# Optimization experiments

Hardware: AMD Instinct MI355X
Metric: run time of the kernel (lower is better)

Reference implementation:

```python
import jax, jax.numpy as jnp
import numpy as np

B, N, C = 128, 197, 768   # batch, tokens (14*14 + cls), embed dim
H = 12                    # attention heads, head_dim = 64
OUT = 32                  # hard-coded mlp out_features
CH_H = 14                 # channel-attention heads
CN = 196                  # channel-attention token dim (14*14)
MLP_HID = int(C * 4.0)    # 3072
CMLP_HID = int(OUT * 4.0) # 128
EPS = 1e-5


def _ln(x, g, b):
    m = x.mean(-1, keepdims=True)
    v = ((x - m) ** 2).mean(-1, keepdims=True)
    return (x - m) * jax.lax.rsqrt(v + EPS) * g + b


def setup_inputs() -> dict:
    key = jax.random.key(0)
    ks = jax.random.split(key, 24)
    W = lambda k, sh: (jax.random.normal(k, sh, jnp.float32) * 0.02)
    return {
        "x": jax.random.normal(ks[0], (B, N, C), jnp.float32),
        # block 1: norm1 + token attention
        "g1": jnp.ones((C,), jnp.float32), "b1": jnp.zeros((C,), jnp.float32),
        "w_qkv": W(ks[1], (3 * C, C)),                     # qkv_bias=False
        "w_proj": W(ks[2], (C, C)), "b_proj": jnp.zeros((C,), jnp.float32),
        # block 2: norm2 + mlp (768 -> 3072 -> 32), NOT residual
        "g2": jnp.ones((C,), jnp.float32), "b2": jnp.zeros((C,), jnp.float32),
        "w_fc1": W(ks[3], (MLP_HID, C)), "b_fc1": jnp.zeros((MLP_HID,), jnp.float32),
        "w_fc2": W(ks[4], (OUT, MLP_HID)), "b_fc2": jnp.zeros((OUT,), jnp.float32),
        # block 3: norm3 + channel attention (over 196 spatial positions)
        "g3": jnp.ones((OUT,), jnp.float32), "b3": jnp.zeros((OUT,), jnp.float32),
        "w_cqkv": W(ks[5], (3 * CN, CN)),                  # qkv_bias=False
        "w_cproj": W(ks[6], (CN, CN)), "b_cproj": jnp.zeros((CN,), jnp.float32),
        # block 4: norm4 + channel mlp (32 -> 128 -> 32)
        "g4": jnp.ones((OUT,), jnp.float32), "b4": jnp.zeros((OUT,), jnp.float32),
        "w_cfc1": W(ks[7], (CMLP_HID, OUT)), "b_cfc1": jnp.zeros((CMLP_HID,), jnp.float32),
        "w_cfc2": W(ks[8], (OUT, CMLP_HID)), "b_cfc2": jnp.zeros((OUT,), jnp.float32),
    }


def reference(x, g1, b1, w_qkv, w_proj, b_proj,
              g2, b2, w_fc1, b_fc1, w_fc2, b_fc2,
              g3, b3, w_cqkv, w_cproj, b_cproj,
              g4, b4, w_cfc1, b_cfc1, w_cfc2, b_cfc2):
    Bz, Nn, Cc = x.shape
    hd = Cc // H  # 64

    # --- token attention (residual) ---
    h = _ln(x, g1, b1)
    qkv = (h @ w_qkv.T).reshape(Bz, Nn, 3, H, hd).transpose(2, 0, 3, 1, 4)
    q, k, v = qkv[0], qkv[1], qkv[2]                       # [B,H,N,hd]
    a = jax.nn.softmax(jnp.einsum('bhqd,bhkd->bhqk', q, k) * (hd ** -0.5), axis=-1)
    o = jnp.einsum('bhqk,bhkd->bhqd', a, v).transpose(0, 2, 1, 3).reshape(Bz, Nn, Cc)
    x = x + (o @ w_proj.T + b_proj)

    # --- mlp 768->3072->32, NO residual (matches original forward) ---
    h = _ln(x, g2, b2)
    x = jax.nn.gelu(h @ w_fc1.T + b_fc1, approximate=False) @ w_fc2.T + b_fc2  # [B,N,32]

    # --- channel attention (residual); N==197 path, no interleave averaging ---
    h = _ln(x, g3, b3)
    cls = h[:, :1, :]                                      # [B,1,32]
    t = h[:, 1:, :].transpose(0, 2, 1)                     # [B,32,196]
    chd = CN // CH_H  # 14
    cqkv = (t @ w_cqkv.T).reshape(Bz, OUT, 3, CH_H, chd).transpose(2, 0, 3, 1, 4)
    cq, ck, cv = cqkv[0], cqkv[1], cqkv[2]                 # [B,14,32,14]
    ca = jax.nn.softmax(jnp.einsum('bhqd,bhkd->bhqk', cq, ck) * (chd ** -0.5), axis=-1)
    co = jnp.einsum('bhqk,bhkd->bhqd', ca, cv).transpose(0, 2, 1, 3).reshape(Bz, OUT, CN)
    co = co @ w_cproj.T + b_cproj                          # [B,32,196]
    x = x + jnp.concatenate([cls, co.transpose(0, 2, 1)], axis=1)

    # --- channel mlp 32->128->32 (residual) ---
    h = _ln(x, g4, b4)
    x = x + (jax.nn.gelu(h @ w_cfc1.T + b_cfc1, approximate=False) @ w_cfc2.T + b_cfc2)
    return x
```

## Files before the change

kernel.cpp:

```cpp
#include <hip/hip_runtime.h>
#include <hip/hip_bf16.h>

typedef unsigned short u16;
typedef __hip_bfloat16 bf16;
typedef __attribute__((ext_vector_type(8))) short bf16x8;
typedef __attribute__((ext_vector_type(4))) float f32x4;

#define B_   128
#define N_   197
#define C_   768
#define H_   12
#define HD_  64
#define T_   (B_*N_)
#define MH_  3072
#define OUT_ 32
#define CN_  196
#define CHH_ 14
#define KP_  224
#define CSZ_ (B_*CHH_*32*14)

__device__ __forceinline__ float bfu2f(u16 x){ union{unsigned u; float f;} v; v.u=((unsigned)x)<<16; return v.f; }
__device__ __forceinline__ bf16  f2bf(float f){ return __float2bfloat16(f); }
__device__ __forceinline__ u16   f2bfu(float f){ union{bf16 h; u16 u;} c; c.h=__float2bfloat16(f); return c.u; }
__device__ __forceinline__ float gelu_f(float x){ return 0.5f*x*(1.0f+erff(x*0.70710678118654752f)); }

__device__ __forceinline__ void gl_lds16(const u16* g, u16* l){
  __builtin_amdgcn_global_load_lds((const __attribute__((address_space(1))) void*)g,
                                   (__attribute__((address_space(3))) void*)l, 16, 0, 0);
}

__global__ __launch_bounds__(256) void write_code_kernel(float* out, int n, float code){
  int i = blockIdx.x*256 + threadIdx.x;
  if (i < n) out[i] = code;
}

template<bool F32IN>
__global__ __launch_bounds__(256) void ln768_kernel(const void* __restrict__ xv,
    const float* __restrict__ g, const float* __restrict__ b, bf16* __restrict__ out)
{
  int row = blockIdx.x;
  int tid = threadIdx.x;
  float v0, v1, v2;
  if (F32IN){
    const float* xr = (const float*)xv + (size_t)row*C_;
    v0 = xr[tid]; v1 = xr[tid+256]; v2 = xr[tid+512];
  } else {
    const u16* xr = (const u16*)xv + (size_t)row*C_;
    v0 = bfu2f(xr[tid]); v1 = bfu2f(xr[tid+256]); v2 = bfu2f(xr[tid+512]);
  }
  __shared__ float red[4];
  int lane = tid & 63, wave = tid >> 6;
  float s = v0+v1+v2;
  #pragma unroll
  for (int off=32; off>0; off>>=1) s += __shfl_xor(s, off);
  if (lane==0) red[wave]=s;
  __syncthreads();
  float mean = (red[0]+red[1]+red[2]+red[3]) * (1.0f/C_);
  float d0=v0-mean, d1=v1-mean, d2=v2-mean;
  float q = d0*d0+d1*d1+d2*d2;
  #pragma unroll
  for (int off=32; off>0; off>>=1) q += __shfl_xor(q, off);
  __syncthreads();
  if (lane==0) red[wave]=q;
  __syncthreads();
  float var = (red[0]+red[1]+red[2]+red[3]) * (1.0f/C_);
  float r = rsqrtf(var + 1e-5f);
  bf16* orow = out + (size_t)row*C_;
  orow[tid]     = f2bf(d0*r*g[tid]     + b[tid]);
  orow[tid+256] = f2bf(d1*r*g[tid+256] + b[tid+256]);
  orow[tid+512] = f2bf(d2*r*g[tid+512] + b[tid+512]);
}

__global__ __launch_bounds__(256) void ln32_kernel(const float* __restrict__ x,
    const float* __restrict__ g, const float* __restrict__ b, float* __restrict__ out)
{
  int i = blockIdx.x*256 + threadIdx.x;
  int c = i & 31;
  float v = x[i];
  float s = v;
  #pragma unroll
  for (int off=16; off>0; off>>=1) s += __shfl_xor(s, off, 32);
  float mean = s * (1.0f/32);
  float d = v - mean;
  float q = d*d;
  #pragma unroll
  for (int off=16; off>0; off>>=1) q += __shfl_xor(q, off, 32);
  float r = rsqrtf(q*(1.0f/32) + 1e-5f);
  out[i] = d*r*g[c] + b[c];
}

__global__ __launch_bounds__(256) void packw_bf16(const float* __restrict__ w,
    u16* __restrict__ dst, int n)
{
  int i = (blockIdx.x*256 + threadIdx.x)*4;
  if (i >= n) return;
  float4 v = *(const float4*)(w + i);
  ushort4 o; o.x=f2bfu(v.x); o.y=f2bfu(v.y); o.z=f2bfu(v.z); o.w=f2bfu(v.w);
  *(ushort4*)(dst + i) = o;
}

__global__ __launch_bounds__(256) void init_x3_kernel(const float* __restrict__ bias,
    float* __restrict__ x3)
{
  int i = blockIdx.x*256 + threadIdx.x;
  x3[i] = bias[i & 31];
}

template<int MODE, bool WB16>
__global__ __launch_bounds__(256) void gemm128(
    const u16* __restrict__ A, const void* __restrict__ Wsrc,
    const float* __restrict__ bias, const float* __restrict__ resid,
    bf16* __restrict__ outb,
    bf16* __restrict__ q_out, bf16* __restrict__ k_out, bf16* __restrict__ v_out,
    int Nn, int K)
{
  __shared__ __align__(16) u16 As[128*32];
  __shared__ __align__(16) u16 Bs[128*32];
  const int tid  = threadIdx.x;
  const int wave = tid >> 6, lane = tid & 63;
  const int quad = lane >> 4, l16 = lane & 15;
  const int wr = wave >> 1, wc = wave & 1;
  const int m0 = blockIdx.x * 128;
  const int n0 = blockIdx.y * 128;
  const int rs = tid >> 2;
  const int kc = (tid & 3) << 3;

  const u16* aA0 = A + (size_t)(m0 + rs)*K + kc;
  const u16* aA1 = aA0 + (size_t)64*K;
  const u16*  wB0 = WB16 ? ((const u16*)Wsrc + (size_t)(n0 + rs)*K + kc) : nullptr;
  const float* wF0 = WB16 ? nullptr : ((const float*)Wsrc + (size_t)(n0 + rs)*K + kc);

  u16* AsW = As + (size_t)wave*512;
  u16* BsW = Bs + (size_t)wave*512;

  f32x4 acc[4][4] = {};

  for (int k0 = 0; k0 < K; k0 += 32){
    gl_lds16(aA0 + k0, AsW);
    gl_lds16(aA1 + k0, AsW + 2048);
    if (WB16){
      gl_lds16(wB0 + k0, BsW);
      gl_lds16(wB0 + (size_t)64*K + k0, BsW + 2048);
    } else {
      float4 w0 = *(const float4*)(wF0 + k0);
      float4 w1 = *(const float4*)(wF0 + k0 + 4);
      const float* wF1 = wF0 + (size_t)64*K;
      float4 w2 = *(const float4*)(wF1 + k0);
      float4 w3 = *(const float4*)(wF1 + k0 + 4);
      ushort4 b0; b0.x=f2bfu(w0.x); b0.y=f2bfu(w0.y); b0.z=f2bfu(w0.z); b0.w=f2bfu(w0.w);
      ushort4 b1; b1.x=f2bfu(w1.x); b1.y=f2bfu(w1.y); b1.z=f2bfu(w1.z); b1.w=f2bfu(w1.w);
      ushort4 b2; b2.x=f2bfu(w2.x); b2.y=f2bfu(w2.y); b2.z=f2bfu(w2.z); b2.w=f2bfu(w2.w);
      ushort4 b3; b3.x=f2bfu(w3.x); b3.y=f2bfu(w3.y); b3.z=f2bfu(w3.z); b3.w=f2bfu(w3.w);
      *(ushort4*)&Bs[rs*32 + kc]        = b0;
      *(ushort4*)&Bs[rs*32 + kc + 4]    = b1;
      *(ushort4*)&Bs[(rs+64)*32 + kc]   = b2;
      *(ushort4*)&Bs[(rs+64)*32 + kc+4] = b3;
    }
    __syncthreads();
    bf16x8 af[4], bfr[4];
    #pragma unroll
    for (int i=0;i<4;i++) af[i]  = *(const bf16x8*)&As[(wr*64 + i*16 + l16)*32 + quad*8];
    #pragma unroll
    for (int j=0;j<4;j++) bfr[j] = *(const bf16x8*)&Bs[(wc*64 + j*16 + l16)*32 + quad*8];
    #pragma unroll
    for (int i=0;i<4;i++)
      #pragma unroll
      for (int j=0;j<4;j++)
        acc[i][j] = __builtin_amdgcn_mfma_f32_16x16x32_bf16(af[i], bfr[j], acc[i][j], 0, 0, 0);
    __syncthreads();
  }

  #pragma unroll
  for (int i=0;i<4;i++){
    #pragma unroll
    for (int j=0;j<4;j++){
      #pragma unroll
      for (int r=0;r<4;r++){
        int m = m0 + wr*64 + i*16 + quad*4 + r;
        int c = n0 + wc*64 + j*16 + l16;
        float v = acc[i][j][r];
        if (MODE==0){
          int bb = m / N_;
          int n  = m - bb*N_;
          int sec = c / C_;
          int rem = c - sec*C_;
          int hh  = rem >> 6;
          int d   = rem & 63;
          bf16* dst = (sec==0) ? q_out : (sec==1) ? k_out : v_out;
          dst[(((size_t)bb*H_ + hh)*N_ + n)*HD_ + d] = f2bf(v);
        } else if (MODE==1){
          size_t idx = (size_t)m*Nn + c;
          outb[idx] = f2bf(v + bias[c] + resid[idx]);
        } else {
          outb[(size_t)m*Nn + c] = f2bf(gelu_f(v + bias[c]));
        }
      }
    }
  }
}

template<int MODE, bool WB16>
__global__ __launch_bounds__(256) void gemm_mfma(
    const u16* __restrict__ A, const void* __restrict__ Wsrc,
    const float* __restrict__ bias, const float* __restrict__ resid,
    bf16* __restrict__ outb, float* __restrict__ outf,
    bf16* __restrict__ q_out, bf16* __restrict__ k_out, bf16* __restrict__ v_out,
    int M, int Nn, int K, int wld, int astride)
{
  __shared__ __align__(16) u16 As[64][32];
  __shared__ __align__(16) u16 Bs[64][32];
  const int tid  = threadIdx.x;
  const int wave = tid >> 6, lane = tid & 63;
  const int quad = lane >> 4, l16 = lane & 15;
  const int m0 = blockIdx.x * 64;
  const int n0 = (MODE==6) ? 0 : blockIdx.y * 64;
  const int kst = (MODE==6) ? blockIdx.y * K : 0;
  const int rs = tid >> 2;
  const int kc = (tid & 3) << 3;
  const u16* arow = A + (size_t)(m0 + rs)*astride + kst + kc;
  const bool wvalid = (n0 + rs) < Nn;

  f32x4 acc[4] = {};

  for (int k0 = 0; k0 < K; k0 += 32){
    *(uint4*)&As[rs][kc] = *(const uint4*)(arow + k0);
    if (WB16){
      const u16* wrow = (const u16*)Wsrc + (size_t)(n0 + rs)*wld + kst + kc;
      uint4 wv = make_uint4(0u,0u,0u,0u);
      if (wvalid) wv = *(const uint4*)(wrow + k0);
      *(uint4*)&Bs[rs][kc] = wv;
    } else {
      const float* wrow = (const float*)Wsrc + (size_t)(n0 + rs)*wld + kst + kc;
      float4 w0 = make_float4(0.f,0.f,0.f,0.f), w1 = w0;
      if (wvalid){ w0 = *(const float4*)(wrow + k0); w1 = *(const float4*)(wrow + k0 + 4); }
      ushort4 b0; b0.x=f2bfu(w0.x); b0.y=f2bfu(w0.y); b0.z=f2bfu(w0.z); b0.w=f2bfu(w0.w);
      ushort4 b1; b1.x=f2bfu(w1.x); b1.y=f2bfu(w1.y); b1.z=f2bfu(w1.z); b1.w=f2bfu(w1.w);
      *(ushort4*)&Bs[rs][kc]   = b0;
      *(ushort4*)&Bs[rs][kc+4] = b1;
    }
    __syncthreads();
    bf16x8 af = *(const bf16x8*)&As[wave*16 + l16][quad*8];
    #pragma unroll
    for (int nb=0; nb<4; nb++){
      bf16x8 bfr = *(const bf16x8*)&Bs[nb*16 + l16][quad*8];
      acc[nb] = __builtin_amdgcn_mfma_f32_16x16x32_bf16(af, bfr, acc[nb], 0, 0, 0);
    }
    __syncthreads();
  }

  #pragma unroll
  for (int nb=0; nb<4; nb++){
    #pragma unroll
    for (int r=0; r<4; r++){
      int m = m0 + wave*16 + quad*4 + r;
      int c = n0 + nb*16 + l16;
      float v = acc[nb][r];
      if (MODE==3){
        if (c < Nn) outf[(size_t)m*Nn + c] = v + bias[c];
      } else if (MODE==4){
        if (c < Nn) outf[(size_t)m*Nn + c] += v;
      } else if (MODE==6){
        if (c < Nn) atomicAdd(&outf[(size_t)m*Nn + c], v);
      } else if (MODE==5){
        if (c < Nn){
          int bb = m >> 5, oo = m & 31;
          int sec = c / CN_;
          int rem = c - sec*CN_;
          int hh  = rem / 14;
          int d   = rem - hh*14;
          outf[(size_t)sec*CSZ_ + (((size_t)bb*CHH_ + hh)*32 + oo)*14 + d] = v;
        }
      }
    }
  }
}

__global__ __launch_bounds__(256) void attn_kernel(const u16* __restrict__ q,
    const u16* __restrict__ k, const u16* __restrict__ v, bf16* __restrict__ o)
{
  __shared__ __align__(16) u16 VtS[64*208];
  __shared__ __align__(16) u16 PsS[4*16*208];
  int bh = blockIdx.x, b = bh / H_, hh = bh - b*H_;
  int tid = threadIdx.x, wave = tid >> 6, lane = tid & 63;
  int quad = lane >> 4, l16 = lane & 15;
  const u16* qb = q + (size_t)bh*N_*HD_;
  const u16* kb = k + (size_t)bh*N_*HD_;
  const u16* vb = v + (size_t)bh*N_*HD_;
  for (int idx = tid; idx < N_*HD_; idx += 256){
    int j = idx >> 6, d = idx & 63;
    VtS[(d*208 + j) ^ ((d&7)<<3)] = vb[idx];
  }
  for (int idx = tid; idx < 64*11; idx += 256){
    int d = idx / 11, j = 197 + (idx - d*11);
    VtS[(d*208 + j) ^ ((d&7)<<3)] = 0;
  }
  __syncthreads();

  u16* PsW = PsS + wave*16*208;

  for (int g = wave; g < 13; g += 4){
    int r0 = g*16;
    int qrow = r0 + l16;
    int qr = (qrow < N_) ? qrow : 0;
    bf16x8 aq0 = *(const bf16x8*)(qb + (size_t)qr*HD_ + quad*8);
    bf16x8 aq1 = *(const bf16x8*)(qb + (size_t)qr*HD_ + 32 + quad*8);
    f32x4 s[13];
    #pragma unroll
    for (int nb = 0; nb < 13; nb++){
      int krow = nb*16 + l16;
      int kr = (krow < N_) ? krow : 0;
      bf16x8 bk0 = *(const bf16x8*)(kb + (size_t)kr*HD_ + quad*8);
      bf16x8 bk1 = *(const bf16x8*)(kb + (size_t)kr*HD_ + 32 + quad*8);
      f32x4 t = {};
      t = __builtin_amdgcn_mfma_f32_16x16x32_bf16(aq0, bk0, t, 0, 0, 0);
      t = __builtin_amdgcn_mfma_f32_16x16x32_bf16(aq1, bk1, t, 0, 0, 0);
      s[nb] = t;
    }
    #pragma unroll
    for (int nb = 0; nb < 13; nb++){
      bool colok = (nb*16 + l16) < N_;
      #pragma unroll
      for (int r = 0; r < 4; r++)
        s[nb][r] = colok ? s[nb][r]*0.125f : -1e30f;
    }
    #pragma unroll
    for (int r = 0; r < 4; r++){
      float m = s[0][r];
      #pragma unroll
      for (int nb = 1; nb < 13; nb++) m = fmaxf(m, s[nb][r]);
      m = fmaxf(m, __shfl_xor(m, 1));
      m = fmaxf(m, __shfl_xor(m, 2));
      m = fmaxf(m, __shfl_xor(m, 4));
      m = fmaxf(m, __shfl_xor(m, 8));
      float su = 0.f;
      #pragma unroll
      for (int nb = 0; nb < 13; nb++){
        float p = expf(s[nb][r] - m);
        s[nb][r] = p; su += p;
      }
      su += __shfl_xor(su, 1);
      su += __shfl_xor(su, 2);
      su += __shfl_xor(su, 4);
      su += __shfl_xor(su, 8);
      float inv = 1.0f/su;
      #pragma unroll
      for (int nb = 0; nb < 13; nb++) s[nb][r] *= inv;
    }
    #pragma unroll
    for (int nb = 0; nb < 13; nb++)
      #pragma unroll
      for (int r = 0; r < 4; r++){
        int row = quad*4 + r;
        PsW[(row*208 + nb*16 + l16) ^ ((row&7)<<3)] = f2bfu(s[nb][r]);
      }
    __threadfence_block();
    f32x4 oa[4] = {};
    #pragma unroll
    for (int ks = 0; ks < 7; ks++){
      int col = ks*32 + quad*8;
      bool ok = (col < 208);
      int ccol = ok ? col : 0;
      bf16x8 ap = *(const bf16x8*)&PsW[(l16*208 + ccol) ^ ((l16&7)<<3)];
      if (!ok) ap = (bf16x8){0,0,0,0,0,0,0,0};
      #pragma unroll
      for (int nd = 0; nd < 4; nd++){
        bf16x8 bv = *(const bf16x8*)&VtS[((nd*16 + l16)*208 + ccol) ^ ((l16&7)<<3)];
        oa[nd] = __builtin_amdgcn_mfma_f32_16x16x32_bf16(ap, bv, oa[nd], 0, 0, 0);
      }
    }
    #pragma unroll
    for (int nd = 0; nd < 4; nd++)
      #pragma unroll
      for (int r = 0; r < 4; r++){
        int qi = r0 + quad*4 + r;
        if (qi < N_)
          o[((size_t)b*N_ + qi)*C_ + hh*HD_ + nd*16 + l16] = f2bf(oa[nd][r]);
      }
    __threadfence_block();
  }
}

__global__ __launch_bounds__(256) void pack_tall_kernel(const float* __restrict__ h3,
    u16* __restrict__ tall)
{
  int idx = blockIdx.x*256 + threadIdx.x;
  if (idx >= 4096*KP_) return;
  int row = idx / KP_, kk = idx - row*KP_;
  int b = row >> 5, oo = row & 31;
  float v = (kk < CN_) ? h3[((size_t)b*N_ + 1 + kk)*32 + oo] : 0.f;
  tall[idx] = f2bfu(v);
}

__global__ __launch_bounds__(256) void pack_w_kernel(const float* __restrict__ w,
    u16* __restrict__ dst, int rows, int kreal)
{
  int idx = blockIdx.x*256 + threadIdx.x;
  if (idx >= rows*KP_) return;
  int r = idx / KP_, kk = idx - r*KP_;
  dst[idx] = (kk < kreal) ? f2bfu(w[(size_t)r*kreal + kk]) : (u16)0;
}

__global__ __launch_bounds__(256) void pack_co_kernel(const float* __restrict__ co,
    u16* __restrict__ dst)
{
  int idx = blockIdx.x*256 + threadIdx.x;
  if (idx >= 4096*KP_) return;
  int row = idx / KP_, kk = idx - row*KP_;
  dst[idx] = (kk < CN_) ? f2bfu(co[(size_t)row*CN_ + kk]) : (u16)0;
}

__global__ __launch_bounds__(64) void cattn_kernel(const float* __restrict__ cq,
    const float* __restrict__ ck, const float* __restrict__ cv, float* __restrict__ co)
{
  __shared__ __align__(16) float qs[32*15], ks_[32*15], vs[32*15], ps[32*34];
  int bh = blockIdx.x;
  int b  = bh / CHH_;
  int hh = bh - b*CHH_;
  int lane = threadIdx.x;
  const float* qb = cq + (size_t)bh*448;
  const float* kb = ck + (size_t)bh*448;
  const float* vb = cv + (size_t)bh*448;
  for (int idx=lane; idx<448; idx+=64){
    int o = idx/14, d = idx - o*14;
    qs[o*15+d] = qb[idx]; ks_[o*15+d] = kb[idx]; vs[o*15+d] = vb[idx];
  }
  __syncthreads();
  int o = lane & 31, half = lane >> 5;
  const float scale = 0.2672612419124244f;
  float sc[16]; float mx = -1e30f;
  #pragma unroll
  for (int jj=0; jj<16; jj++){
    int j = half*16 + jj;
    float a = 0.f;
    #pragma unroll
    for (int d=0; d<14; d++) a += qs[o*15+d]*ks_[j*15+d];
    sc[jj] = a*scale;
    mx = fmaxf(mx, sc[jj]);
  }
  mx = fmaxf(mx, __shfl_xor(mx, 32));
  float sum = 0.f;
  #pragma unroll
  for (int jj=0; jj<16; jj++){ sc[jj] = expf(sc[jj]-mx); sum += sc[jj]; }
  sum += __shfl_xor(sum, 32);
  float inv = 1.0f/sum;
  #pragma unroll
  for (int jj=0; jj<16; jj++) ps[o*34 + half*16 + jj] = sc[jj]*inv;
  __syncthreads();
  #pragma unroll
  for (int dd=0; dd<7; dd++){
    int d = half*7 + dd;
    float acc = 0.f;
    #pragma unroll
    for (int j=0; j<32; j++) acc += ps[o*34+j]*vs[j*15+d];
    co[((size_t)b*32 + o)*CN_ + hh*14 + d] = acc;
  }
}

__global__ __launch_bounds__(256) void concat_add_kernel(const float* __restrict__ x3,
    const float* __restrict__ h3, const float* __restrict__ co2, float* __restrict__ x4)
{
  int i = blockIdx.x*256 + threadIdx.x;
  int c = i & 31;
  int row = i >> 5;
  int b = row / N_;
  int r = row - b*N_;
  float add = (r==0) ? h3[i] : co2[((size_t)b*32 + c)*CN_ + (r-1)];
  x4[i] = x3[i] + add;
}

__global__ __launch_bounds__(256) void cfc1_kernel(const float* __restrict__ h4,
    const float* __restrict__ w, const float* __restrict__ bias, float* __restrict__ chid)
{
  int idx = blockIdx.x*256 + threadIdx.x;
  int m = idx >> 7, j = idx & 127;
  const float* hr = h4 + (size_t)m*32;
  const float* wr = w + (size_t)j*32;
  float acc = bias[j];
  #pragma unroll
  for (int kk=0; kk<32; kk++) acc += hr[kk]*wr[kk];
  chid[idx] = gelu_f(acc);
}

__global__ __launch_bounds__(256) void cfc2_kernel(const float* __restrict__ chid,
    const float* __restrict__ w, const float* __restrict__ bias,
    const float* __restrict__ x4, float* __restrict__ out)
{
  int idx = blockIdx.x*256 + threadIdx.x;
  int m = idx >> 5, j = idx & 31;
  const float* cr = chid + (size_t)m*128;
  const float* wr = w + (size_t)j*128;
  float acc = bias[j];
  #pragma unroll
  for (int kk=0; kk<128; kk++) acc += cr[kk]*wr[kk];
  out[idx] = x4[idx] + acc;
}

extern "C" void kernel_launch(void* const* d_in, const int* in_sizes, int n_in,
                              void* d_out, int out_size, void* d_ws, size_t ws_size,
                              hipStream_t stream)
{
  const int NIN = 23;
  static const int dsz[NIN] = {19365888,768,768,1769472,589824,768,768,768,2359296,
                               3072,98304,32,32,32,115248,38416,196,32,32,4096,128,4096,32};
  static const int a2d[NIN] = {2,7,13,18,20,22,16,9,11,5,1,6,12,17,19,21,15,14,8,10,4,3,0};

  float* dout = (float*)d_out;
  int ogrid = (out_size + 255)/256;

  const float* in[NIN];
  bool dict_ok = (n_in == NIN);
  if (dict_ok) for (int i=0;i<NIN;i++) if (in_sizes[i] != dsz[i]) { dict_ok=false; break; }
  if (dict_ok){
    for (int i=0;i<NIN;i++) in[i] = (const float*)d_in[i];
  } else {
    bool alpha_ok = (n_in == NIN);
    if (alpha_ok) for (int i=0;i<NIN;i++) if (in_sizes[i] != dsz[a2d[i]]) { alpha_ok=false; break; }
    if (alpha_ok){
      for (int i=0;i<NIN;i++) in[a2d[i]] = (const float*)d_in[i];
    } else {
      write_code_kernel<<<ogrid, 256, 0, stream>>>(dout, out_size, 5000.f + (float)n_in);
      return;
    }
  }

  const float* x      = in[0];
  const float* g1     = in[1];
  const float* b1     = in[2];
  const float* w_qkv  = in[3];
  const float* w_proj = in[4];
  const float* b_proj = in[5];
  const float* g2     = in[6];
  const float* b2     = in[7];
  const float* w_fc1  = in[8];
  const float* b_fc1  = in[9];
  const float* w_fc2  = in[10];
  const float* b_fc2  = in[11];
  const float* g3     = in[12];
  const float* b3     = in[13];
  const float* w_cqkv = in[14];
  const float* w_cproj= in[15];
  const float* b_cproj= in[16];
  const float* g4     = in[17];
  const float* b4     = in[18];
  const float* w_cfc1 = in[19];
  const float* b_cfc1 = in[20];
  const float* w_cfc2 = in[21];
  const float* b_cfc2 = in[22];

  char* ws = (char*)d_ws;
  const size_t TC2 = (size_t)T_*C_*2;
  const size_t NEED = 4*TC2 + 4096;
  if (ws_size < NEED){
    write_code_kernel<<<ogrid, 256, 0, stream>>>(dout, out_size,
        7000.f + (float)(ws_size >> 20));
    return;
  }

  bf16* h_buf   = (bf16*)(ws);
  bf16* o_buf   = (bf16*)(ws);
  bf16* q_buf   = (bf16*)(ws + TC2);
  bf16* k_buf   = (bf16*)(ws + 2*TC2);
  bf16* v_buf   = (bf16*)(ws + 3*TC2);
  bf16* x2_buf  = (bf16*)(ws + TC2);
  bf16* hidh    = (bf16*)(ws + 2*TC2);
  float* x3     = (float*)(ws + TC2);
  char* sm = ws + 2*TC2;
  float* h3  = (float*)sm; sm += (size_t)T_*32*4;
  float* cq  = (float*)sm; sm += (size_t)CSZ_*4;
  float* ck  = (float*)sm; sm += (size_t)CSZ_*4;
  float* cv  = (float*)sm; sm += (size_t)CSZ_*4;
  float* co  = (float*)sm; sm += (size_t)B_*32*CN_*4;
  float* co2 = (float*)sm; sm += (size_t)B_*32*CN_*4;
  float* x4  = (float*)sm; sm += (size_t)T_*32*4;
  float* h4  = (float*)sm; sm += (size_t)T_*32*4;
  float* chid = (float*)sm;
  u16* tall  = (u16*)(ws);
  u16* wcq_b = (u16*)(ws + 2*1024*1024);
  u16* co_b  = (u16*)(ws + 3*1024*1024);
  u16* wcp_b = (u16*)(ws + 5*1024*1024);

  u16* wqkv_b  = (u16*)(ws + 4*TC2 + 4096);
  u16* wproj_b = wqkv_b  + (size_t)2304*C_;
  u16* wfc1_b  = wproj_b + (size_t)C_*C_;
  const size_t WPACK = ((size_t)2304*C_ + (size_t)C_*C_ + (size_t)MH_*C_)*2;
  const bool packed = (ws_size >= NEED + WPACK);

  if (packed){
    packw_bf16<<<(2304*C_/4+255)/256, 256, 0, stream>>>(w_qkv,  wqkv_b,  2304*C_);
    packw_bf16<<<(C_*C_/4+255)/256,  256, 0, stream>>>(w_proj, wproj_b, C_*C_);
    packw_bf16<<<(MH_*C_/4+255)/256, 256, 0, stream>>>(w_fc1,  wfc1_b,  MH_*C_);
  }

  ln768_kernel<true><<<T_, 256, 0, stream>>>(x, g1, b1, h_buf);
  if (packed)
    gemm128<0,true><<<dim3(T_/128, 2304/128), 256, 0, stream>>>((const u16*)h_buf,
        wqkv_b, nullptr, nullptr, nullptr, q_buf, k_buf, v_buf, 2304, C_);
  else
    gemm128<0,false><<<dim3(T_/128, 2304/128), 256, 0, stream>>>((const u16*)h_buf,
        w_qkv, nullptr, nullptr, nullptr, q_buf, k_buf, v_buf, 2304, C_);
  attn_kernel<<<B_*H_, 256, 0, stream>>>((const u16*)q_buf, (const u16*)k_buf,
      (const u16*)v_buf, o_buf);
  if (packed)
    gemm128<1,true><<<dim3(T_/128, C_/128), 256, 0, stream>>>((const u16*)o_buf,
        wproj_b, b_proj, x, x2_buf, nullptr, nullptr, nullptr, C_, C_);
  else
    gemm128<1,false><<<dim3(T_/128, C_/128), 256, 0, stream>>>((const u16*)o_buf,
        w_proj, b_proj, x, x2_buf, nullptr, nullptr, nullptr, C_, C_);
  ln768_kernel<false><<<T_, 256, 0, stream>>>(x2_buf, g2, b2, h_buf);
  init_x3_kernel<<<(T_*32)/256, 256, 0, stream>>>(b_fc2, x3);
  for (int half=0; half<2; half++){
    if (packed)
      gemm128<2,true><<<dim3(T_/128, 1536/128), 256, 0, stream>>>((const u16*)h_buf,
          wfc1_b + (size_t)half*1536*C_, b_fc1 + half*1536, nullptr,
          hidh, nullptr, nullptr, nullptr, 1536, C_);
    else
      gemm128<2,false><<<dim3(T_/128, 1536/128), 256, 0, stream>>>((const u16*)h_buf,
          w_fc1 + (size_t)half*1536*C_, b_fc1 + half*1536, nullptr,
          hidh, nullptr, nullptr, nullptr, 1536, C_);
    gemm_mfma<6,false><<<dim3(T_/64, 4), 256, 0, stream>>>((const u16*)hidh,
        w_fc2 + (size_t)half*1536, nullptr, nullptr, nullptr, x3,
        nullptr, nullptr, nullptr, T_, OUT_, 384, MH_, 1536);
  }
  ln32_kernel<<<(T_*32)/256, 256, 0, stream>>>(x3, g3, b3, h3);
  pack_tall_kernel<<<(4096*KP_+255)/256, 256, 0, stream>>>(h3, tall);
  pack_w_kernel<<<(588*KP_+255)/256, 256, 0, stream>>>(w_cqkv, wcq_b, 588, CN_);
  gemm_mfma<5,true><<<dim3(4096/64, 10), 256, 0, stream>>>(tall, wcq_b,
      nullptr, nullptr, nullptr, cq, nullptr, nullptr, nullptr, 4096, 588, KP_, KP_, KP_);
  cattn_kernel<<<B_*CHH_, 64, 0, stream>>>(cq, ck, cv, co);
  pack_co_kernel<<<(4096*KP_+255)/256, 256, 0, stream>>>(co, co_b);
  pack_w_kernel<<<(196*KP_+255)/256, 256, 0, stream>>>(w_cproj, wcp_b, CN_, CN_);
  gemm_mfma<3,true><<<dim3(4096/64, 4), 256, 0, stream>>>(co_b, wcp_b,
      b_cproj, nullptr, nullptr, co2, nullptr, nullptr, nullptr, 4096, CN_, KP_, KP_, KP_);
  concat_add_kernel<<<(T_*32)/256, 256, 0, stream>>>(x3, h3, co2, x4);
  ln32_kernel<<<(T_*32)/256, 256, 0, stream>>>(x4, g4, b4, h4);
  cfc1_kernel<<<(T_*128)/256, 256, 0, stream>>>(h4, w_cfc1, b_cfc1, chid);
  cfc2_kernel<<<(T_*32)/256, 256, 0, stream>>>(chid, w_cfc2, b_cfc2, x4, dout);
}
```

Measured before the change: 1.036 ms.

## Double-buffer GEMM LDS, swap grid order, split attention blocks, use exp2

The 128x128 GEMM now keeps two LDS stages, so the next K tile loads while MFMAs run on the current one, which hides global-to-LDS latency. Its grid is transposed so consecutive blocks walk along N and share the same A rows, which should help L2 reuse. Token attention is split into two blocks per (batch, head) for more parallelism, and exp is replaced by exp2 with a pre-scaled log2e, tree reductions and s_setprio around MFMA sections. The cost is twice the GEMM LDS footprint (lower occupancy) and the V transpose being loaded twice per head.

Result: faster. 1.001 ms (-3.4%).

```diff
diff --git a/kernel.cpp b/kernel.cpp
--- a/kernel.cpp
+++ b/kernel.cpp
@@ -114,14 +114,14 @@
     bf16* __restrict__ q_out, bf16* __restrict__ k_out, bf16* __restrict__ v_out,
     int Nn, int K)
 {
-  __shared__ __align__(16) u16 As[128*32];
-  __shared__ __align__(16) u16 Bs[128*32];
+  __shared__ __align__(16) u16 As[2][128*32];
+  __shared__ __align__(16) u16 Bs[2][128*32];
   const int tid  = threadIdx.x;
   const int wave = tid >> 6, lane = tid & 63;
   const int quad = lane >> 4, l16 = lane & 15;
   const int wr = wave >> 1, wc = wave & 1;
-  const int m0 = blockIdx.x * 128;
-  const int n0 = blockIdx.y * 128;
+  const int m0 = blockIdx.y * 128;
+  const int n0 = blockIdx.x * 128;
   const int rs = tid >> 2;
   const int kc = (tid & 3) << 3;
 
@@ -130,12 +130,11 @@
   const u16*  wB0 = WB16 ? ((const u16*)Wsrc + (size_t)(n0 + rs)*K + kc) : nullptr;
   const float* wF0 = WB16 ? nullptr : ((const float*)Wsrc + (size_t)(n0 + rs)*K + kc);
 
-  u16* AsW = As + (size_t)wave*512;
-  u16* BsW = Bs + (size_t)wave*512;
-
   f32x4 acc[4][4] = {};
 
-  for (int k0 = 0; k0 < K; k0 += 32){
+  auto STAGE = [&](int buf, int k0){
+    u16* AsW = As[buf] + (size_t)wave*512;
+    u16* BsW = Bs[buf] + (size_t)wave*512;
     gl_lds16(aA0 + k0, AsW);
     gl_lds16(aA1 + k0, AsW + 2048);
     if (WB16){
@@ -151,23 +150,31 @@
       ushort4 b1; b1.x=f2bfu(w1.x); b1.y=f2bfu(w1.y); b1.z=f2bfu(w1.z); b1.w=f2bfu(w1.w);
       ushort4 b2; b2.x=f2bfu(w2.x); b2.y=f2bfu(w2.y); b2.z=f2bfu(w2.z); b2.w=f2bfu(w2.w);
       ushort4 b3; b3.x=f2bfu(w3.x); b3.y=f2bfu(w3.y); b3.z=f2bfu(w3.z); b3.w=f2bfu(w3.w);
-      *(ushort4*)&Bs[rs*32 + kc]        = b0;
-      *(ushort4*)&Bs[rs*32 + kc + 4]    = b1;
-      *(ushort4*)&Bs[(rs+64)*32 + kc]   = b2;
-      *(ushort4*)&Bs[(rs+64)*32 + kc+4] = b3;
-    }
-    __syncthreads();
+      *(ushort4*)&Bs[buf][rs*32 + kc]        = b0;
+      *(ushort4*)&Bs[buf][rs*32 + kc + 4]    = b1;
+      *(ushort4*)&Bs[buf][(rs+64)*32 + kc]   = b2;
+      *(ushort4*)&Bs[buf][(rs+64)*32 + kc+4] = b3;
+    }
+  };
+
+  STAGE(0, 0);
+  __syncthreads();
+  int cur = 0;
+
+  for (int k0 = 0; k0 < K; k0 += 32){
+    if (k0 + 32 < K) STAGE(cur^1, k0 + 32);
     bf16x8 af[4], bfr[4];
     #pragma unroll
-    for (int i=0;i<4;i++) af[i]  = *(const bf16x8*)&As[(wr*64 + i*16 + l16)*32 + quad*8];
-    #pragma unroll
-    for (int j=0;j<4;j++) bfr[j] = *(const bf16x8*)&Bs[(wc*64 + j*16 + l16)*32 + quad*8];
+    for (int i=0;i<4;i++) af[i]  = *(const bf16x8*)&As[cur][(wr*64 + i*16 + l16)*32 + quad*8];
+    #pragma unroll
+    for (int j=0;j<4;j++) bfr[j] = *(const bf16x8*)&Bs[cur][(wc*64 + j*16 + l16)*32 + quad*8];
     #pragma unroll
     for (int i=0;i<4;i++)
       #pragma unroll
       for (int j=0;j<4;j++)
         acc[i][j] = __builtin_amdgcn_mfma_f32_16x16x32_bf16(af[i], bfr[j], acc[i][j], 0, 0, 0);
     __syncthreads();
+    cur ^= 1;
   }
 
   #pragma unroll
@@ -280,7 +287,9 @@
 {
   __shared__ __align__(16) u16 VtS[64*208];
   __shared__ __align__(16) u16 PsS[4*16*208];
-  int bh = blockIdx.x, b = bh / H_, hh = bh - b*H_;
+  int bid = blockIdx.x;
+  int bh = bid >> 1, sh = bid & 1;
+  int b = bh / H_, hh = bh - b*H_;
   int tid = threadIdx.x, wave = tid >> 6, lane = tid & 63;
   int quad = lane >> 4, l16 = lane & 15;
   const u16* qb = q + (size_t)bh*N_*HD_;
@@ -297,14 +306,18 @@
   __syncthreads();
 
   u16* PsW = PsS + wave*16*208;
-
-  for (int g = wave; g < 13; g += 4){
+  const int gbeg = sh ? 7 : 0;
+  const int gend = sh ? 13 : 7;
+  const float LOG2E = 1.4426950408889634f;
+
+  for (int g = gbeg + wave; g < gend; g += 4){
     int r0 = g*16;
     int qrow = r0 + l16;
     int qr = (qrow < N_) ? qrow : 0;
     bf16x8 aq0 = *(const bf16x8*)(qb + (size_t)qr*HD_ + quad*8);
     bf16x8 aq1 = *(const bf16x8*)(qb + (size_t)qr*HD_ + 32 + quad*8);
     f32x4 s[13];
+    __builtin_amdgcn_s_setprio(1);
     #pragma unroll
     for (int nb = 0; nb < 13; nb++){
       int krow = nb*16 + l16;
@@ -316,28 +329,34 @@
       t = __builtin_amdgcn_mfma_f32_16x16x32_bf16(aq1, bk1, t, 0, 0, 0);
       s[nb] = t;
     }
+    __builtin_amdgcn_s_setprio(0);
     #pragma unroll
     for (int nb = 0; nb < 13; nb++){
       bool colok = (nb*16 + l16) < N_;
       #pragma unroll
       for (int r = 0; r < 4; r++)
-        s[nb][r] = colok ? s[nb][r]*0.125f : -1e30f;
+        s[nb][r] = colok ? s[nb][r]*(0.125f*LOG2E) : -1e30f;
     }
     #pragma unroll
     for (int r = 0; r < 4; r++){
-      float m = s[0][r];
-      #pragma unroll
-      for (int nb = 1; nb < 13; nb++) m = fmaxf(m, s[nb][r]);
+      float m01 = fmaxf(s[0][r], s[1][r]),  m23 = fmaxf(s[2][r], s[3][r]);
+      float m45 = fmaxf(s[4][r], s[5][r]),  m67 = fmaxf(s[6][r], s[7][r]);
+      float m89 = fmaxf(s[8][r], s[9][r]),  mab = fmaxf(s[10][r], s[11][r]);
+      float m = fmaxf(fmaxf(fmaxf(m01,m23), fmaxf(m45,m67)),
+                      fmaxf(fmaxf(m89,mab), s[12][r]));
       m = fmaxf(m, __shfl_xor(m, 1));
       m = fmaxf(m, __shfl_xor(m, 2));
       m = fmaxf(m, __shfl_xor(m, 4));
       m = fmaxf(m, __shfl_xor(m, 8));
-      float su = 0.f;
+      float p[13];
       #pragma unroll
       for (int nb = 0; nb < 13; nb++){
-        float p = expf(s[nb][r] - m);
-        s[nb][r] = p; su += p;
+        p[nb] = __builtin_amdgcn_exp2f(s[nb][r] - m);
+        s[nb][r] = p[nb];
       }
+      float t01=p[0]+p[1], t23=p[2]+p[3], t45=p[4]+p[5], t67=p[6]+p[7];
+      float t89=p[8]+p[9], tab=p[10]+p[11];
+      float su = ((t01+t23)+(t45+t67)) + ((t89+tab)+p[12]);
       su += __shfl_xor(su, 1);
       su += __shfl_xor(su, 2);
       su += __shfl_xor(su, 4);
@@ -355,6 +374,7 @@
       }
     __threadfence_block();
     f32x4 oa[4] = {};
+    __builtin_amdgcn_s_setprio(1);
     #pragma unroll
     for (int ks = 0; ks < 7; ks++){
       int col = ks*32 + quad*8;
@@ -368,6 +388,7 @@
         oa[nd] = __builtin_amdgcn_mfma_f32_16x16x32_bf16(ap, bv, oa[nd], 0, 0, 0);
       }
     }
+    __builtin_amdgcn_s_setprio(0);
     #pragma unroll
     for (int nd = 0; nd < 4; nd++)
       #pragma unroll
@@ -440,7 +461,7 @@
   mx = fmaxf(mx, __shfl_xor(mx, 32));
   float sum = 0.f;
   #pragma unroll
-  for (int jj=0; jj<16; jj++){ sc[jj] = expf(sc[jj]-mx); sum += sc[jj]; }
+  for (int jj=0; jj<16; jj++){ sc[jj] = __expf(sc[jj]-mx); sum += sc[jj]; }
   sum += __shfl_xor(sum, 32);
   float inv = 1.0f/sum;
   #pragma unroll
@@ -593,28 +614,28 @@
 
   ln768_kernel<true><<<T_, 256, 0, stream>>>(x, g1, b1, h_buf);
   if (packed)
-    gemm128<0,true><<<dim3(T_/128, 2304/128), 256, 0, stream>>>((const u16*)h_buf,
+    gemm128<0,true><<<dim3(2304/128, T_/128), 256, 0, stream>>>((const u16*)h_buf,
         wqkv_b, nullptr, nullptr, nullptr, q_buf, k_buf, v_buf, 2304, C_);
   else
-    gemm128<0,false><<<dim3(T_/128, 2304/128), 256, 0, stream>>>((const u16*)h_buf,
+    gemm128<0,false><<<dim3(2304/128, T_/128), 256, 0, stream>>>((const u16*)h_buf,
         w_qkv, nullptr, nullptr, nullptr, q_buf, k_buf, v_buf, 2304, C_);
-  attn_kernel<<<B_*H_, 256, 0, stream>>>((const u16*)q_buf, (const u16*)k_buf,
+  attn_kernel<<<B_*H_*2, 256, 0, stream>>>((const u16*)q_buf, (const u16*)k_buf,
       (const u16*)v_buf, o_buf);
   if (packed)
-    gemm128<1,true><<<dim3(T_/128, C_/128), 256, 0, stream>>>((const u16*)o_buf,
+    gemm128<1,true><<<dim3(C_/128, T_/128), 256, 0, stream>>>((const u16*)o_buf,
         wproj_b, b_proj, x, x2_buf, nullptr, nullptr, nullptr, C_, C_);
   else
-    gemm128<1,false><<<dim3(T_/128, C_/128), 256, 0, stream>>>((const u16*)o_buf,
+    gemm128<1,false><<<dim3(C_/128, T_/128), 256, 0, stream>>>((const u16*)o_buf,
         w_proj, b_proj, x, x2_buf, nullptr, nullptr, nullptr, C_, C_);
   ln768_kernel<false><<<T_, 256, 0, stream>>>(x2_buf, g2, b2, h_buf);
   init_x3_kernel<<<(T_*32)/256, 256, 0, stream>>>(b_fc2, x3);
   for (int half=0; half<2; half++){
     if (packed)
-      gemm128<2,true><<<dim3(T_/128, 1536/128), 256, 0, stream>>>((const u16*)h_buf,
+      gemm128<2,true><<<dim3(1536/128, T_/128), 256, 0, stream>>>((const u16*)h_buf,
           wfc1_b + (size_t)half*1536*C_, b_fc1 + half*1536, nullptr,
           hidh, nullptr, nullptr, nullptr, 1536, C_);
     else
-      gemm128<2,false><<<dim3(T_/128, 1536/128), 256, 0, stream>>>((const u16*)h_buf,
+      gemm128<2,false><<<dim3(1536/128, T_/128), 256, 0, stream>>>((const u16*)h_buf,
           w_fc1 + (size_t)half*1536*C_, b_fc1 + half*1536, nullptr,
           hidh, nullptr, nullptr, nullptr, 1536, C_);
     gemm_mfma<6,false><<<dim3(T_/64, 4), 256, 0, stream>>>((const u16*)hidh,
```
